# Kernel tuning notes

Hardware: AMD Instinct MI355X
Metric: run time of the kernel (lower is better)

## Reference

```python
import jax, jax.numpy as jnp
import numpy as np

NUM_HEADS = 16
EMBED_DIM = 1024
SEQ_LEN = 2048
BATCH = 2


def setup_inputs() -> dict:
    key = jax.random.key(0)
    ks = jax.random.split(key, 7)
    E = EMBED_DIM
    scale = 1.0 / np.sqrt(E)
    return {
        "query": jax.random.normal(ks[0], (SEQ_LEN, BATCH, E), jnp.float32),
        "key": jax.random.normal(ks[1], (SEQ_LEN, BATCH, E), jnp.float32),
        "value": jax.random.normal(ks[2], (SEQ_LEN, BATCH, E), jnp.float32),
        "in_proj_weight": jax.random.normal(ks[3], (3 * E, E), jnp.float32) * scale,
        "in_proj_bias": jnp.zeros((3 * E,), jnp.float32),
        "out_proj_weight": jax.random.normal(ks[4], (E, E), jnp.float32) * scale,
        "out_proj_bias": jnp.zeros((E,), jnp.float32),
    }


def reference(query, key, value, in_proj_weight, in_proj_bias, out_proj_weight, out_proj_bias):
    T, B, E = query.shape
    H = NUM_HEADS
    d = E // H
    scaling = float(d) ** -0.5
    # in-projections: rows [0:E) -> q, [E:2E) -> k, [2E:3E) -> v
    q = query @ in_proj_weight[:E].T + in_proj_bias[:E]
    k = key @ in_proj_weight[E:2 * E].T + in_proj_bias[E:2 * E]
    v = value @ in_proj_weight[2 * E:].T + in_proj_bias[2 * E:]
    q = q * scaling
    # (T, B, E) -> (B*H, T, d)
    q = q.reshape(T, B * H, d).transpose(1, 0, 2)
    k = k.reshape(T, B * H, d).transpose(1, 0, 2)
    v = v.reshape(T, B * H, d).transpose(1, 0, 2)
    S = k.shape[1]
    scores = jnp.einsum('ntd,nsd->nts', q, k)  # (B*H, T, S)
    attn = jax.nn.softmax(scores, axis=-1)
    out = jnp.einsum('nts,nsd->ntd', attn, v)  # (B*H, T, d)
    out = out.transpose(1, 0, 2).reshape(T, B, E)
    out = out @ out_proj_weight.T + out_proj_bias
    attn_avg = attn.reshape(B, H, T, S).sum(axis=1) / H
    return out, attn_avg
```

## Files before the change

kernel.cpp:

```cpp
#include <hip/hip_runtime.h>
#include <math.h>

#define T_LEN 2048
#define BATCH 2
#define EMB 1024
#define NHEAD 16
#define HDIM 64
#define BH (BATCH*NHEAD)
#define MROWS (T_LEN*BATCH)
#define QSCALE (0.125f * 1.4426950408889634f)
#define HEADBUF ((size_t)BH*T_LEN*HDIM)

typedef __attribute__((ext_vector_type(8))) short bf16x8;
typedef __attribute__((ext_vector_type(4))) float f32x4;

#define MFMA16(a,b,c) __builtin_amdgcn_mfma_f32_16x16x32_bf16(a,b,c,0,0,0)

__device__ __forceinline__ short f2bf(float f) {
    union { float f; unsigned u; } v; v.f = f;
    unsigned r = (v.u + 0x7FFFu + ((v.u >> 16) & 1u)) >> 16;
    return (short)(unsigned short)r;
}
__device__ __forceinline__ float bf2f(short s) {
    union { unsigned u; float f; } v; v.u = ((unsigned)(unsigned short)s) << 16;
    return v.f;
}
__device__ __forceinline__ unsigned cvtpk(float a, float b) {
    unsigned r;
    asm("v_cvt_pk_bf16_f32 %0, %1, %2" : "=v"(r) : "v"(a), "v"(b));
    return r;
}
__device__ __forceinline__ void gload16(const void* g, void* l) {
    __builtin_amdgcn_global_load_lds(
        (const __attribute__((address_space(1))) unsigned*)g,
        (__attribute__((address_space(3))) unsigned*)l, 16, 0, 0);
}

__global__ __launch_bounds__(256) void tobf16_kernel(
    const float* __restrict__ q, const float* __restrict__ k,
    const float* __restrict__ v, const float* __restrict__ w,
    const float* __restrict__ wo, short* __restrict__ out)
{
    size_t i8 = ((size_t)blockIdx.x * 256 + threadIdx.x) * 8;
    const float* src; size_t off;
    if (i8 < 12582912) {
        int sel = (int)(i8 >> 22);
        src = (sel == 0) ? q : (sel == 1) ? k : v;
        off = i8 & 4194303;
    } else if (i8 < 15728640) {
        src = w;  off = i8 - 12582912;
    } else {
        src = wo; off = i8 - 15728640;
    }
    float4 f0 = *(const float4*)(src + off);
    float4 f1 = *(const float4*)(src + off + 4);
    bf16x8 o;
    o[0]=f2bf(f0.x); o[1]=f2bf(f0.y); o[2]=f2bf(f0.z); o[3]=f2bf(f0.w);
    o[4]=f2bf(f1.x); o[5]=f2bf(f1.y); o[6]=f2bf(f1.z); o[7]=f2bf(f1.w);
    *(bf16x8*)(out + i8) = o;
}

__global__ __launch_bounds__(256) void inproj_gemm(
    const short* __restrict__ Xq, const short* __restrict__ Xk,
    const short* __restrict__ Xv, const short* __restrict__ Wb,
    const float* __restrict__ bias,
    short* __restrict__ qbuf, short* __restrict__ kbuf, short* __restrict__ vbufT)
{
    const int mBase = blockIdx.x * 128;
    const int nBase = blockIdx.y * 128;
    const int which = nBase >> 10;
    const short* __restrict__ X = (which == 0) ? Xq : (which == 1) ? Xk : Xv;

    __shared__ short Ast[128][64];
    __shared__ short Bst[128][64];

    const int tid  = threadIdx.x;
    const int lane = tid & 63;
    const int w    = tid >> 6;
    const int wr   = w >> 1, wc = w & 1;
    const int lr   = lane & 15, lg = lane >> 4;
    const int srow = tid >> 3;
    const int scol = (tid & 7) * 8;

    f32x4 acc[4][4] = {};

    for (int kb = 0; kb < EMB; kb += 64) {
        __syncthreads();
        #pragma unroll
        for (int j = 0; j < 4; ++j) {
            gload16(X  + (size_t)(mBase + j * 32 + srow) * EMB + kb + scol,
                    (char*)Ast + j * 4096 + w * 1024);
            gload16(Wb + (size_t)(nBase + j * 32 + srow) * EMB + kb + scol,
                    (char*)Bst + j * 4096 + w * 1024);
        }
        __syncthreads();
        #pragma unroll
        for (int ks = 0; ks < 2; ++ks) {
            bf16x8 af[4], bfr[4];
            #pragma unroll
            for (int rg = 0; rg < 4; ++rg)
                af[rg] = *(const bf16x8*)&Ast[wr * 64 + rg * 16 + lr][ks * 32 + lg * 8];
            #pragma unroll
            for (int cg = 0; cg < 4; ++cg)
                bfr[cg] = *(const bf16x8*)&Bst[wc * 64 + cg * 16 + lr][ks * 32 + lg * 8];
            #pragma unroll
            for (int rg = 0; rg < 4; ++rg)
                #pragma unroll
                for (int cg = 0; cg < 4; ++cg)
                    acc[rg][cg] = MFMA16(af[rg], bfr[cg], acc[rg][cg]);
        }
    }

    #pragma unroll
    for (int rg = 0; rg < 4; ++rg) {
        #pragma unroll
        for (int cg = 0; cg < 4; ++cg) {
            int n  = nBase + wc * 64 + cg * 16 + lr;
            int e  = n & 1023;
            int h  = e >> 6, dd = e & 63;
            float bs = bias[n];
            #pragma unroll
            for (int ri = 0; ri < 4; ++ri) {
                int m = mBase + wr * 64 + rg * 16 + lg * 4 + ri;
                int t = m >> 1, b = m & 1;
                float val = acc[rg][cg][ri] + bs;
                short bfv;
                if (which == 0) { bfv = f2bf(val * QSCALE);
                    qbuf[((size_t)(b * NHEAD + h) * T_LEN + t) * HDIM + dd] = bfv; }
                else if (which == 1) { bfv = f2bf(val);
                    kbuf[((size_t)(b * NHEAD + h) * T_LEN + t) * HDIM + dd] = bfv; }
                else { bfv = f2bf(val);
                    vbufT[((size_t)(b * NHEAD + h) * HDIM + dd) * T_LEN + t] = bfv; }
            }
        }
    }
}

__global__ __launch_bounds__(256) void flash_kernel(
    const short* __restrict__ qb, const short* __restrict__ kbuf,
    const short* __restrict__ vbufT, short* __restrict__ h1,
    short* __restrict__ h2, float* __restrict__ mlws)
{
    const int qt = blockIdx.x;
    const int hb = blockIdx.y;

    __shared__ short Kst[64][64];
    __shared__ short Vst[64][64];
    __shared__ short Pst[64][72];

    const int tid  = threadIdx.x;
    const int lane = tid & 63;
    const int w    = tid >> 6;
    const int lr   = lane & 15, lg = lane >> 4;

    bf16x8 qa0, qa1;
    {
        const short* qsrc = qb + ((size_t)hb * T_LEN + qt * 64 + w * 16 + lr) * HDIM;
        qa0 = *(const bf16x8*)(qsrc + lg * 8);
        qa1 = *(const bf16x8*)(qsrc + 32 + lg * 8);
    }

    const short* kbase = kbuf  + (size_t)hb * T_LEN * HDIM;
    const short* vbase = vbufT + (size_t)hb * HDIM * T_LEN;

    const int krow = lane >> 3;
    const int kc16 = (lane & 7) ^ krow;
    const int rb0 = ((0 + lg) ^ (lr & 7)) * 16;
    const int rb1 = ((4 + lg) ^ (lr & 7)) * 16;

    float l_r = 0.f;
    f32x4 o_acc[4] = {};

    for (int st = 0; st < T_LEN / 64; ++st) {
        __syncthreads();
        #pragma unroll
        for (int it = 0; it < 2; ++it) {
            int r = (w * 2 + it) * 8 + krow;
            gload16(kbase + (size_t)(st * 64 + r) * HDIM + kc16 * 8,
                    (char*)Kst + (w * 2 + it) * 1024);
            gload16(vbase + (size_t)r * T_LEN + st * 64 + kc16 * 8,
                    (char*)Vst + (w * 2 + it) * 1024);
        }
        __syncthreads();

        f32x4 sc[4] = {};
        #pragma unroll
        for (int sg = 0; sg < 4; ++sg) {
            const char* krowp = (const char*)Kst + (sg * 16 + lr) * 128;
            bf16x8 kf0 = *(const bf16x8*)(krowp + rb0);
            bf16x8 kf1 = *(const bf16x8*)(krowp + rb1);
            sc[sg] = MFMA16(kf0, qa0, sc[sg]);
            sc[sg] = MFMA16(kf1, qa1, sc[sg]);
        }

        float p[4][4];
        #pragma unroll
        for (int sg = 0; sg < 4; ++sg)
            #pragma unroll
            for (int ri = 0; ri < 4; ++ri) {
                p[sg][ri] = exp2f(sc[sg][ri]);
                l_r += p[sg][ri];
            }

        #pragma unroll
        for (int sg = 0; sg < 4; ++sg) {
            uint2 pk;
            pk.x = cvtpk(p[sg][0], p[sg][1]);
            pk.y = cvtpk(p[sg][2], p[sg][3]);
            *(uint2*)&Pst[w * 16 + lr][sg * 16 + lg * 4] = pk;
        }

        #pragma unroll
        for (int ks = 0; ks < 2; ++ks) {
            bf16x8 pa = *(const bf16x8*)&Pst[w * 16 + lr][ks * 32 + lg * 8];
            #pragma unroll
            for (int dsub = 0; dsub < 4; ++dsub) {
                const char* vrowp = (const char*)Vst + (dsub * 16 + lr) * 128;
                bf16x8 vf = *(const bf16x8*)(vrowp + (ks ? rb1 : rb0));
                o_acc[dsub] = MFMA16(pa, vf, o_acc[dsub]);
            }
        }
    }

    float lsum = l_r;
    lsum += __shfl_xor(lsum, 16);
    lsum += __shfl_xor(lsum, 32);
    float inv = 1.0f / lsum;
    float invq[4];
    #pragma unroll
    for (int ri = 0; ri < 4; ++ri) invq[ri] = __shfl(inv, lg * 20 + ri);
    #pragma unroll
    for (int ri = 0; ri < 4; ++ri) {
        int row = qt * 64 + w * 16 + lg * 4 + ri;
        #pragma unroll
        for (int dsub = 0; dsub < 4; ++dsub) {
            float x = o_acc[dsub][ri] * invq[ri];
            size_t idx = ((size_t)hb * T_LEN + row) * HDIM + dsub * 16 + lr;
            short a = f2bf(x);
            h1[idx] = a;
            h2[idx] = f2bf(x - bf2f(a));
        }
    }
    if (lg == 0) {
        int row = qt * 64 + w * 16 + lr;
        mlws[(size_t)hb * T_LEN + row] = __log2f(lsum);
    }
}

__global__ __launch_bounds__(256) void avg_kernel(
    const short* __restrict__ qbuf, const short* __restrict__ kbuf,
    const float* __restrict__ mlws, float* __restrict__ attn_avg)
{
    const int st = blockIdx.x;
    const int qt = blockIdx.y;
    const int b  = blockIdx.z;

    __shared__ short K2[2][2][64][64];

    const int tid  = threadIdx.x;
    const int lane = tid & 63;
    const int w    = tid >> 6;
    const int lr   = lane & 15, lg = lane >> 4;
    const int srow = tid >> 3;
    const int scol = (tid & 7) * 8;

    f32x4 acc[4] = {};

    #pragma unroll
    for (int hh = 0; hh < 2; ++hh) {
        int hb0 = b * NHEAD + hh;
        #pragma unroll
        for (int j = 0; j < 2; ++j)
            gload16(kbuf + ((size_t)hb0 * T_LEN + st * 64 + j * 32 + srow) * HDIM + scol,
                    (char*)K2[0][hh] + j * 4096 + w * 1024);
    }
    __syncthreads();

    int cur = 0;
    for (int rnd = 0; rnd < 8; ++rnd) {
        if (rnd + 1 < 8) {
            #pragma unroll
            for (int hh = 0; hh < 2; ++hh) {
                int hbn = b * NHEAD + (rnd + 1) * 2 + hh;
                #pragma unroll
                for (int j = 0; j < 2; ++j)
                    gload16(kbuf + ((size_t)hbn * T_LEN + st * 64 + j * 32 + srow) * HDIM + scol,
                            (char*)K2[cur ^ 1][hh] + j * 4096 + w * 1024);
            }
        }
        #pragma unroll
        for (int hh = 0; hh < 2; ++hh) {
            int hb = b * NHEAD + rnd * 2 + hh;
            const short* qsrc = qbuf + ((size_t)hb * T_LEN + qt * 64 + w * 16 + lr) * HDIM;
            bf16x8 qa0 = *(const bf16x8*)(qsrc + lg * 8);
            bf16x8 qa1 = *(const bf16x8*)(qsrc + 32 + lg * 8);

            f32x4 sc[4] = {};
            #pragma unroll
            for (int sg = 0; sg < 4; ++sg) {
                bf16x8 kf0 = *(const bf16x8*)&K2[cur][hh][sg * 16 + lr][lg * 8];
                bf16x8 kf1 = *(const bf16x8*)&K2[cur][hh][sg * 16 + lr][32 + lg * 8];
                sc[sg] = MFMA16(qa0, kf0, sc[sg]);
                sc[sg] = MFMA16(qa1, kf1, sc[sg]);
            }

            #pragma unroll
            for (int ri = 0; ri < 4; ++ri) {
                int row = qt * 64 + w * 16 + lg * 4 + ri;
                float ml = mlws[(size_t)hb * T_LEN + row];
                #pragma unroll
                for (int sg = 0; sg < 4; ++sg)
                    acc[sg][ri] += exp2f(sc[sg][ri] - ml);
            }
        }
        __syncthreads();
        cur ^= 1;
    }

    const float invH = 1.0f / (float)NHEAD;
    #pragma unroll
    for (int ri = 0; ri < 4; ++ri) {
        int row = qt * 64 + w * 16 + lg * 4 + ri;
        #pragma unroll
        for (int sg = 0; sg < 4; ++sg)
            attn_avg[((size_t)b * T_LEN + row) * T_LEN + st * 64 + sg * 16 + lr] =
                acc[sg][ri] * invH;
    }
}

__global__ __launch_bounds__(256) void outproj_gemm(
    const short* __restrict__ h1, const short* __restrict__ h2,
    const short* __restrict__ Wob, const float* __restrict__ bo,
    float* __restrict__ out)
{
    const int mBase = blockIdx.x * 128;
    const int nBase = blockIdx.y * 128;

    __shared__ short A1st[128][64];
    __shared__ short A2st[128][64];
    __shared__ short Bst [128][64];

    const int tid  = threadIdx.x;
    const int lane = tid & 63;
    const int w    = tid >> 6;
    const int wr   = w >> 1, wc = w & 1;
    const int lr   = lane & 15, lg = lane >> 4;
    const int srow = tid >> 3;
    const int scol = (tid & 7) * 8;

    f32x4 acc[4][4] = {};

    for (int kb = 0; kb < EMB; kb += 64) {
        const int h = kb >> 6;
        __syncthreads();
        #pragma unroll
        for (int j = 0; j < 4; ++j) {
            int m = mBase + j * 32 + srow;
            int t = m >> 1, b = m & 1;
            size_t aoff = ((size_t)(b * NHEAD + h) * T_LEN + t) * HDIM + scol;
            gload16(h1 + aoff, (char*)A1st + j * 4096 + w * 1024);
            gload16(h2 + aoff, (char*)A2st + j * 4096 + w * 1024);
            gload16(Wob + (size_t)(nBase + j * 32 + srow) * EMB + kb + scol,
                    (char*)Bst + j * 4096 + w * 1024);
        }
        __syncthreads();
        #pragma unroll
        for (int ks = 0; ks < 2; ++ks) {
            bf16x8 a1[4], a2[4], bfr[4];
            #pragma unroll
            for (int rg = 0; rg < 4; ++rg) {
                a1[rg] = *(const bf16x8*)&A1st[wr * 64 + rg * 16 + lr][ks * 32 + lg * 8];
                a2[rg] = *(const bf16x8*)&A2st[wr * 64 + rg * 16 + lr][ks * 32 + lg * 8];
            }
            #pragma unroll
            for (int cg = 0; cg < 4; ++cg)
                bfr[cg] = *(const bf16x8*)&Bst[wc * 64 + cg * 16 + lr][ks * 32 + lg * 8];
            #pragma unroll
            for (int rg = 0; rg < 4; ++rg)
                #pragma unroll
                for (int cg = 0; cg < 4; ++cg) {
                    acc[rg][cg] = MFMA16(a1[rg], bfr[cg], acc[rg][cg]);
                    acc[rg][cg] = MFMA16(a2[rg], bfr[cg], acc[rg][cg]);
                }
        }
    }

    #pragma unroll
    for (int rg = 0; rg < 4; ++rg) {
        #pragma unroll
        for (int cg = 0; cg < 4; ++cg) {
            int n = nBase + wc * 64 + cg * 16 + lr;
            float bs = bo[n];
            #pragma unroll
            for (int ri = 0; ri < 4; ++ri) {
                int m = mBase + wr * 64 + rg * 16 + lg * 4 + ri;
                out[(size_t)m * EMB + n] = acc[rg][cg][ri] + bs;
            }
        }
    }
}

extern "C" void kernel_launch(void* const* d_in, const int* in_sizes, int n_in,
                              void* d_out, int out_size, void* d_ws, size_t ws_size,
                              hipStream_t stream)
{
    const float* query = (const float*)d_in[0];
    const float* key   = (const float*)d_in[1];
    const float* value = (const float*)d_in[2];
    const float* ipw   = (const float*)d_in[3];
    const float* ipb   = (const float*)d_in[4];
    const float* opw   = (const float*)d_in[5];
    const float* opb   = (const float*)d_in[6];

    short* qb  = (short*)d_ws;
    short* kb  = qb + HEADBUF;
    short* vbT = kb + HEADBUF;
    short* h1  = vbT + HEADBUF;
    short* h2  = h1 + HEADBUF;
    short* xvb = h2 + HEADBUF;
    short* wbf = xvb + HEADBUF;
    short* wob = wbf + (size_t)3 * EMB * EMB;
    float* mlws = (float*)(wob + (size_t)EMB * EMB);

    float* out      = (float*)d_out;
    float* attn_avg = out + (size_t)MROWS * EMB;

    tobf16_kernel<<<8192, 256, 0, stream>>>(query, key, value, ipw, opw, h1);
    inproj_gemm  <<<dim3(MROWS / 128, 3 * EMB / 128), 256, 0, stream>>>(
        h1, h2, xvb, wbf, ipb, qb, kb, vbT);
    flash_kernel <<<dim3(T_LEN / 64, BH),             256, 0, stream>>>(
        qb, kb, vbT, h1, h2, mlws);
    avg_kernel   <<<dim3(T_LEN / 64, T_LEN / 64, BATCH), 256, 0, stream>>>(
        qb, kb, mlws, attn_avg);
    outproj_gemm <<<dim3(MROWS / 128, EMB / 128),     256, 0, stream>>>(
        h1, h2, wob, opb, out);
}
```

Measured before the change: 224.2 us.

## Double-buffer in-projection GEMM with swizzled LDS and remap blocks for XCD locality

The in-projection GEMM now uses double-buffered shared memory with K-chunks of 32, so the next tile's global loads are issued before the MFMAs on the current tile. A single barrier per iteration replaces two. Shared-memory chunks are XOR-swizzled to reduce LDS bank conflicts on fragment reads. Both GEMMs also remap the linear block index so consecutive blocks land on the same XCD (stride-8 interleave), which is meant to improve L2 reuse; the cost is more loop iterations and added index arithmetic.

```diff
diff --git a/kernel.cpp b/kernel.cpp
--- a/kernel.cpp
+++ b/kernel.cpp
@@ -66,49 +66,64 @@
     const float* __restrict__ bias,
     short* __restrict__ qbuf, short* __restrict__ kbuf, short* __restrict__ vbufT)
 {
-    const int mBase = blockIdx.x * 128;
-    const int nBase = blockIdx.y * 128;
+    const int lin = blockIdx.y * 32 + blockIdx.x;
+    const int tl  = (lin & 7) * 96 + (lin >> 3);
+    const int mBase = (tl & 31) * 128;
+    const int nBase = (tl >> 5) * 128;
     const int which = nBase >> 10;
     const short* __restrict__ X = (which == 0) ? Xq : (which == 1) ? Xk : Xv;
 
-    __shared__ short Ast[128][64];
-    __shared__ short Bst[128][64];
+    __shared__ short Ast[2][128][32];
+    __shared__ short Bst[2][128][32];
 
     const int tid  = threadIdx.x;
     const int lane = tid & 63;
     const int w    = tid >> 6;
     const int wr   = w >> 1, wc = w & 1;
     const int lr   = lane & 15, lg = lane >> 4;
-    const int srow = tid >> 3;
-    const int scol = (tid & 7) * 8;
+
+    const int srow = lane >> 2;
+    const int schk = (lane & 3) ^ ((lane >> 3) & 3);
+    const int fchk = (lg ^ ((lr >> 1) & 3)) * 16;
 
     f32x4 acc[4][4] = {};
 
-    for (int kb = 0; kb < EMB; kb += 64) {
-        __syncthreads();
-        #pragma unroll
-        for (int j = 0; j < 4; ++j) {
-            gload16(X  + (size_t)(mBase + j * 32 + srow) * EMB + kb + scol,
-                    (char*)Ast + j * 4096 + w * 1024);
-            gload16(Wb + (size_t)(nBase + j * 32 + srow) * EMB + kb + scol,
-                    (char*)Bst + j * 4096 + w * 1024);
-        }
-        __syncthreads();
-        #pragma unroll
-        for (int ks = 0; ks < 2; ++ks) {
-            bf16x8 af[4], bfr[4];
-            #pragma unroll
-            for (int rg = 0; rg < 4; ++rg)
-                af[rg] = *(const bf16x8*)&Ast[wr * 64 + rg * 16 + lr][ks * 32 + lg * 8];
+    #pragma unroll
+    for (int j = 0; j < 2; ++j) {
+        int r = j * 64 + w * 16 + srow;
+        gload16(X  + (size_t)(mBase + r) * EMB + schk * 8,
+                (char*)Ast[0] + j * 4096 + w * 1024);
+        gload16(Wb + (size_t)(nBase + r) * EMB + schk * 8,
+                (char*)Bst[0] + j * 4096 + w * 1024);
+    }
+    __syncthreads();
+
+    int cur = 0;
+    for (int kb = 0; kb < EMB; kb += 32) {
+        if (kb + 32 < EMB) {
+            #pragma unroll
+            for (int j = 0; j < 2; ++j) {
+                int r = j * 64 + w * 16 + srow;
+                gload16(X  + (size_t)(mBase + r) * EMB + kb + 32 + schk * 8,
+                        (char*)Ast[cur ^ 1] + j * 4096 + w * 1024);
+                gload16(Wb + (size_t)(nBase + r) * EMB + kb + 32 + schk * 8,
+                        (char*)Bst[cur ^ 1] + j * 4096 + w * 1024);
+            }
+        }
+        bf16x8 af[4], bfr[4];
+        #pragma unroll
+        for (int rg = 0; rg < 4; ++rg)
+            af[rg] = *(const bf16x8*)((char*)Ast[cur] + (wr * 64 + rg * 16 + lr) * 64 + fchk);
+        #pragma unroll
+        for (int cg = 0; cg < 4; ++cg)
+            bfr[cg] = *(const bf16x8*)((char*)Bst[cur] + (wc * 64 + cg * 16 + lr) * 64 + fchk);
+        #pragma unroll
+        for (int rg = 0; rg < 4; ++rg)
             #pragma unroll
             for (int cg = 0; cg < 4; ++cg)
-                bfr[cg] = *(const bf16x8*)&Bst[wc * 64 + cg * 16 + lr][ks * 32 + lg * 8];
-            #pragma unroll
-            for (int rg = 0; rg < 4; ++rg)
-                #pragma unroll
-                for (int cg = 0; cg < 4; ++cg)
-                    acc[rg][cg] = MFMA16(af[rg], bfr[cg], acc[rg][cg]);
-        }
+                acc[rg][cg] = MFMA16(af[rg], bfr[cg], acc[rg][cg]);
+        __syncthreads();
+        cur ^= 1;
     }
 
     #pragma unroll
@@ -333,8 +348,10 @@
     const short* __restrict__ Wob, const float* __restrict__ bo,
     float* __restrict__ out)
 {
-    const int mBase = blockIdx.x * 128;
-    const int nBase = blockIdx.y * 128;
+    const int lin = blockIdx.y * 32 + blockIdx.x;
+    const int tl  = (lin & 7) * 32 + (lin >> 3);
+    const int mBase = (tl & 31) * 128;
+    const int nBase = (tl >> 5) * 128;
 
     __shared__ short A1st[128][64];
     __shared__ short A2st[128][64];
```

Measured after the change: 226.8 us. Within noise of the previous version (+1.1%).
